# Optimization experiments

Measured on AMD Instinct MI355X. Metric: run time of the kernel, lower is better.

The kernel has to match this reference:

```python
import jax, jax.numpy as jnp
import numpy as np

TEMPERATURE = 8.0  # init arg


def setup_inputs() -> dict:
    key = jax.random.key(0)
    kq, kv, kk = jax.random.split(key, 3)
    B, W, H, C, M, D = 4, 64, 64, 256, 32, 32
    q = jax.random.normal(kq, (B, W, H, M, D), dtype=jnp.float32)
    v = jax.random.normal(kv, (B, W, H, C, M), dtype=jnp.float32)
    k = jax.random.normal(kk, (B, W, H, D, 1), dtype=jnp.float32)
    return {"q": q, "v": v, "k": k}


def reference(q, v, k):
    # attn = (q / T) @ k : [B,W,H,M,1]
    attn = jnp.matmul(q / TEMPERATURE, k)
    # softmax over dim=-2 (the query/slot axis M), NOT the usual key axis
    attn = jax.nn.softmax(attn, axis=-2)
    # v @ attn : [B,W,H,C,M] @ [B,W,H,M,1] -> [B,W,H,C,1] -> squeeze -> [B,W,H,C]
    out = jnp.matmul(v, attn)[..., 0]
    # permute(0,3,1,2) -> [B,C,W,H]; the subsequent .view is a no-op reshape
    return jnp.transpose(out, (0, 3, 1, 2))
```

## Files before the change

### kernel.cpp

```cpp
#include <hip/hip_runtime.h>


#define TEMP_INV 0.125f
#define G 16

typedef float f4 __attribute__((ext_vector_type(4)));

__global__ __launch_bounds__(256) void sdpa_kernel(
    const float* __restrict__ q,
    const float* __restrict__ v,
    const float* __restrict__ k,
    float* __restrict__ out)
{
    const int t   = threadIdx.x;
    const int p0  = blockIdx.x * G;
    const int b   = p0 >> 12;
    const int wh0 = p0 & 4095;

    __shared__ float s_k[G * 32];
    __shared__ float s_logit[G * 32];
    __shared__ float s_attn[G * 32];
    __shared__ float s_out[256 * 17];

    if (t < 128) {
        f4 k4 = ((const f4*)k)[p0 * 8 + t];
        k4 *= TEMP_INV;
        ((f4*)s_k)[t] = k4;
    }
    __syncthreads();

    const int j = t & 7;
    const int m = t >> 3;
    #pragma unroll 4
    for (int g = 0; g < G; ++g) {
        const f4 q4 = __builtin_nontemporal_load((const f4*)q + (p0 + g) * 256 + t);
        const float* kg = &s_k[g * 32 + j * 4];
        float partial = q4.x * kg[0] + q4.y * kg[1] + q4.z * kg[2] + q4.w * kg[3];
        partial += __shfl_down(partial, 4, 8);
        partial += __shfl_down(partial, 2, 8);
        partial += __shfl_down(partial, 1, 8);
        if (j == 0) s_logit[g * 32 + m] = partial;
    }
    __syncthreads();

    {
        const int mm = t & 31;
        #pragma unroll
        for (int r = 0; r < 2; ++r) {
            const int g = (t >> 5) + r * 8;
            float l = s_logit[g * 32 + mm];
            float mx = l;
            #pragma unroll
            for (int off = 16; off; off >>= 1)
                mx = fmaxf(mx, __shfl_xor(mx, off, 32));
            float e = __expf(l - mx);
            float s = e;
            #pragma unroll
            for (int off = 16; off; off >>= 1)
                s += __shfl_xor(s, off, 32);
            s_attn[g * 32 + mm] = e / s;
        }
    }
    __syncthreads();

    const int c0 = t >> 3;
    #pragma unroll 2
    for (int g = 0; g < G; ++g) {
        const float* ag = &s_attn[g * 32 + j * 4];
        const float a0 = ag[0], a1 = ag[1], a2 = ag[2], a3 = ag[3];
        const f4* v4p = (const f4*)v + (size_t)(p0 + g) * 2048;
        float acc[8];
        #pragma unroll
        for (int i = 0; i < 8; ++i) {
            const f4 v4 = __builtin_nontemporal_load(v4p + t + 256 * i);
            acc[i] = v4.x * a0 + v4.y * a1 + v4.z * a2 + v4.w * a3;
        }
        #pragma unroll
        for (int i = 0; i < 8; ++i) {
            acc[i] += __shfl_down(acc[i], 4, 8);
            acc[i] += __shfl_down(acc[i], 2, 8);
            acc[i] += __shfl_down(acc[i], 1, 8);
        }
        if (j == 0) {
            #pragma unroll
            for (int i = 0; i < 8; ++i)
                s_out[(c0 + 32 * i) * 17 + g] = acc[i];
        }
    }
    __syncthreads();

    {
        const int c  = t >> 2;
        const int gc = t & 3;
        #pragma unroll
        for (int i = 0; i < 4; ++i) {
            const int cc = c + 64 * i;
            const float* so = &s_out[cc * 17 + gc * 4];
            f4 o4 = { so[0], so[1], so[2], so[3] };
            __builtin_nontemporal_store(
                o4, (f4*)out + (size_t)(b * 256 + cc) * 1024 + (wh0 >> 2) + gc);
        }
    }
}

extern "C" void kernel_launch(void* const* d_in, const int* in_sizes, int n_in,
                              void* d_out, int out_size, void* d_ws, size_t ws_size,
                              hipStream_t stream) {
    const float* q = (const float*)d_in[0];
    const float* v = (const float*)d_in[1];
    const float* k = (const float*)d_in[2];
    float* out = (float*)d_out;
    sdpa_kernel<<<16384 / G, 256, 0, stream>>>(q, v, k, out);
}
```

Baseline: 683.5 us.

## Split fused kernel into attention kernel and channel-split PV kernel

Splits the single fused kernel into two launches. The first computes softmax attention weights and writes them to workspace. The second reads v with the grid split four ways over channels, so it launches four times as many blocks with a smaller per-thread load footprint and less shared memory. This aims to raise occupancy and memory parallelism on the dominant v stream, at the cost of an extra launch and a small round trip of attention weights through global memory.

```diff
diff --git a/kernel.cpp b/kernel.cpp
--- a/kernel.cpp
+++ b/kernel.cpp
@@ -3,24 +3,22 @@
 
 #define TEMP_INV 0.125f
 #define G 16
+#define CSPLIT 4
+#define CB (256 / CSPLIT)
 
 typedef float f4 __attribute__((ext_vector_type(4)));
 
-__global__ __launch_bounds__(256) void sdpa_kernel(
+__global__ __launch_bounds__(256) void attn_kernel(
     const float* __restrict__ q,
-    const float* __restrict__ v,
     const float* __restrict__ k,
-    float* __restrict__ out)
+    float* __restrict__ attn_out)
 {
-    const int t   = threadIdx.x;
-    const int p0  = blockIdx.x * G;
-    const int b   = p0 >> 12;
-    const int wh0 = p0 & 4095;
+    const int t  = threadIdx.x;
+    const int p0 = blockIdx.x * G;
 
     __shared__ float s_k[G * 32];
     __shared__ float s_logit[G * 32];
     __shared__ float s_attn[G * 32];
-    __shared__ float s_out[256 * 17];
 
     if (t < 128) {
         f4 k4 = ((const f4*)k)[p0 * 8 + t];
@@ -63,28 +61,49 @@
     }
     __syncthreads();
 
-    const int c0 = t >> 3;
-    #pragma unroll 2
+    if (t < 128)
+        ((f4*)attn_out)[p0 * 8 + t] = ((f4*)s_attn)[t];
+}
+
+__global__ __launch_bounds__(256) void pv_kernel(
+    const float* __restrict__ v,
+    const float* __restrict__ attn,
+    float* __restrict__ out)
+{
+    const int t   = threadIdx.x;
+    const int blk = blockIdx.x;
+    const int p0  = (blk >> 2) * G;
+    const int c0  = (blk & 3) * CB;
+    const int b   = p0 >> 12;
+    const int wh0 = p0 & 4095;
+
+    __shared__ float s_attn[G * 32];
+    __shared__ float s_out[CB * 17];
+
+    if (t < 128)
+        ((f4*)s_attn)[t] = ((const f4*)attn)[p0 * 8 + t];
+    __syncthreads();
+
+    const int j  = t & 7;
+    const int cr = t >> 3;
+    #pragma unroll 4
     for (int g = 0; g < G; ++g) {
         const float* ag = &s_attn[g * 32 + j * 4];
         const float a0 = ag[0], a1 = ag[1], a2 = ag[2], a3 = ag[3];
-        const f4* v4p = (const f4*)v + (size_t)(p0 + g) * 2048;
-        float acc[8];
-        #pragma unroll
-        for (int i = 0; i < 8; ++i) {
-            const f4 v4 = __builtin_nontemporal_load(v4p + t + 256 * i);
-            acc[i] = v4.x * a0 + v4.y * a1 + v4.z * a2 + v4.w * a3;
-        }
-        #pragma unroll
-        for (int i = 0; i < 8; ++i) {
-            acc[i] += __shfl_down(acc[i], 4, 8);
-            acc[i] += __shfl_down(acc[i], 2, 8);
-            acc[i] += __shfl_down(acc[i], 1, 8);
-        }
+        const f4* v4p = (const f4*)v + (size_t)(p0 + g) * 2048 + c0 * 8;
+        f4 v40 = __builtin_nontemporal_load(v4p + t);
+        f4 v41 = __builtin_nontemporal_load(v4p + t + 256);
+        float acc0 = v40.x * a0 + v40.y * a1 + v40.z * a2 + v40.w * a3;
+        float acc1 = v41.x * a0 + v41.y * a1 + v41.z * a2 + v41.w * a3;
+        acc0 += __shfl_down(acc0, 4, 8);
+        acc0 += __shfl_down(acc0, 2, 8);
+        acc0 += __shfl_down(acc0, 1, 8);
+        acc1 += __shfl_down(acc1, 4, 8);
+        acc1 += __shfl_down(acc1, 2, 8);
+        acc1 += __shfl_down(acc1, 1, 8);
         if (j == 0) {
-            #pragma unroll
-            for (int i = 0; i < 8; ++i)
-                s_out[(c0 + 32 * i) * 17 + g] = acc[i];
+            s_out[cr * 17 + g]        = acc0;
+            s_out[(cr + 32) * 17 + g] = acc1;
         }
     }
     __syncthreads();
@@ -92,14 +111,10 @@
     {
         const int c  = t >> 2;
         const int gc = t & 3;
-        #pragma unroll
-        for (int i = 0; i < 4; ++i) {
-            const int cc = c + 64 * i;
-            const float* so = &s_out[cc * 17 + gc * 4];
-            f4 o4 = { so[0], so[1], so[2], so[3] };
-            __builtin_nontemporal_store(
-                o4, (f4*)out + (size_t)(b * 256 + cc) * 1024 + (wh0 >> 2) + gc);
-        }
+        const float* so = &s_out[c * 17 + gc * 4];
+        f4 o4 = { so[0], so[1], so[2], so[3] };
+        __builtin_nontemporal_store(
+            o4, (f4*)out + (size_t)(b * 256 + c0 + c) * 1024 + (wh0 >> 2) + gc);
     }
 }
 
@@ -110,5 +125,8 @@
     const float* v = (const float*)d_in[1];
     const float* k = (const float*)d_in[2];
     float* out = (float*)d_out;
-    sdpa_kernel<<<16384 / G, 256, 0, stream>>>(q, v, k, out);
+    float* attn = (float*)d_ws;
+
+    attn_kernel<<<16384 / G, 256, 0, stream>>>(q, k, attn);
+    pv_kernel<<<(16384 / G) * CSPLIT, 256, 0, stream>>>(v, attn, out);
 }
```

Measured after the change: 689.5 us. About the same (+0.9%).

## Split into attention and PV kernels with per-thread full-row dot products

Applied to the files above, without the earlier changes.

Splits the fused kernel into two launches. The first computes the softmax attention weights into workspace, and the second computes the V-by-attention product. Each thread now loads a full 32-float row (8 consecutive f4) and does the whole dot product itself, which removes the shuffle reductions. The group per block also shrinks from 16 to 8 positions. In exchange there is an extra launch and a global round trip for the attention weights, loads are no longer coalesced across threads (each thread strides 128 bytes), and the nontemporal loads are dropped.

```diff
diff --git a/kernel.cpp b/kernel.cpp
--- a/kernel.cpp
+++ b/kernel.cpp
@@ -2,104 +2,95 @@
 
 
 #define TEMP_INV 0.125f
-#define G 16
 
 typedef float f4 __attribute__((ext_vector_type(4)));
 
-__global__ __launch_bounds__(256) void sdpa_kernel(
+__global__ __launch_bounds__(256) void attn_kernel(
     const float* __restrict__ q,
-    const float* __restrict__ v,
     const float* __restrict__ k,
-    float* __restrict__ out)
+    float* __restrict__ attn_out)
 {
-    const int t   = threadIdx.x;
-    const int p0  = blockIdx.x * G;
-    const int b   = p0 >> 12;
-    const int wh0 = p0 & 4095;
+    const int t  = threadIdx.x;
+    const int p0 = blockIdx.x * 8;
 
-    __shared__ float s_k[G * 32];
-    __shared__ float s_logit[G * 32];
-    __shared__ float s_attn[G * 32];
-    __shared__ float s_out[256 * 17];
+    __shared__ float s_k[8 * 32];
 
-    if (t < 128) {
+    if (t < 64) {
         f4 k4 = ((const f4*)k)[p0 * 8 + t];
         k4 *= TEMP_INV;
         ((f4*)s_k)[t] = k4;
     }
     __syncthreads();
 
-    const int j = t & 7;
-    const int m = t >> 3;
-    #pragma unroll 4
-    for (int g = 0; g < G; ++g) {
-        const f4 q4 = __builtin_nontemporal_load((const f4*)q + (p0 + g) * 256 + t);
-        const float* kg = &s_k[g * 32 + j * 4];
-        float partial = q4.x * kg[0] + q4.y * kg[1] + q4.z * kg[2] + q4.w * kg[3];
-        partial += __shfl_down(partial, 4, 8);
-        partial += __shfl_down(partial, 2, 8);
-        partial += __shfl_down(partial, 1, 8);
-        if (j == 0) s_logit[g * 32 + m] = partial;
+    const int g = t >> 5;
+    const int m = t & 31;
+
+    const f4* qp = (const f4*)q + ((size_t)(p0 + g) * 256 + m * 8);
+    const f4* kp = (const f4*)&s_k[g * 32];
+
+    float l = 0.f;
+    #pragma unroll
+    for (int i = 0; i < 8; ++i) {
+        const f4 qq = qp[i];
+        const f4 kk = kp[i];
+        l += qq.x * kk.x + qq.y * kk.y + qq.z * kk.z + qq.w * kk.w;
+    }
+
+    float mx = l;
+    #pragma unroll
+    for (int off = 16; off; off >>= 1)
+        mx = fmaxf(mx, __shfl_xor(mx, off, 32));
+    float e = __expf(l - mx);
+    float s = e;
+    #pragma unroll
+    for (int off = 16; off; off >>= 1)
+        s += __shfl_xor(s, off, 32);
+
+    attn_out[p0 * 32 + t] = e / s;
+}
+
+__global__ __launch_bounds__(256) void pv_kernel(
+    const float* __restrict__ v,
+    const float* __restrict__ attn,
+    float* __restrict__ out)
+{
+    const int t   = threadIdx.x;
+    const int p0  = blockIdx.x * 8;
+    const int b   = p0 >> 12;
+    const int wh0 = p0 & 4095;
+
+    __shared__ float s_attn[8 * 32];
+    __shared__ float s_out[256 * 9];
+
+    if (t < 64)
+        ((f4*)s_attn)[t] = ((const f4*)attn)[p0 * 8 + t];
+    __syncthreads();
+
+    const f4* vbase = (const f4*)v + ((size_t)p0 * 2048 + t * 8);
+    #pragma unroll
+    for (int g = 0; g < 8; ++g) {
+        const f4* vp = vbase + g * 2048;
+        const f4* ap = (const f4*)&s_attn[g * 32];
+        float a = 0.f;
+        #pragma unroll
+        for (int i = 0; i < 8; ++i) {
+            const f4 vv = vp[i];
+            const f4 aa = ap[i];
+            a += vv.x * aa.x + vv.y * aa.y + vv.z * aa.z + vv.w * aa.w;
+        }
+        s_out[t * 9 + g] = a;
     }
     __syncthreads();
 
-    {
-        const int mm = t & 31;
-        #pragma unroll
-        for (int r = 0; r < 2; ++r) {
-            const int g = (t >> 5) + r * 8;
-            float l = s_logit[g * 32 + mm];
-            float mx = l;
-            #pragma unroll
-            for (int off = 16; off; off >>= 1)
-                mx = fmaxf(mx, __shfl_xor(mx, off, 32));
-            float e = __expf(l - mx);
-            float s = e;
-            #pragma unroll
-            for (int off = 16; off; off >>= 1)
-                s += __shfl_xor(s, off, 32);
-            s_attn[g * 32 + mm] = e / s;
-        }
-    }
-    __syncthreads();
-
-    const int c0 = t >> 3;
-    #pragma unroll 2
-    for (int g = 0; g < G; ++g) {
-        const float* ag = &s_attn[g * 32 + j * 4];
-        const float a0 = ag[0], a1 = ag[1], a2 = ag[2], a3 = ag[3];
-        const f4* v4p = (const f4*)v + (size_t)(p0 + g) * 2048;
-        float acc[8];
-        #pragma unroll
-        for (int i = 0; i < 8; ++i) {
-            const f4 v4 = __builtin_nontemporal_load(v4p + t + 256 * i);
-            acc[i] = v4.x * a0 + v4.y * a1 + v4.z * a2 + v4.w * a3;
-        }
-        #pragma unroll
-        for (int i = 0; i < 8; ++i) {
-            acc[i] += __shfl_down(acc[i], 4, 8);
-            acc[i] += __shfl_down(acc[i], 2, 8);
-            acc[i] += __shfl_down(acc[i], 1, 8);
-        }
-        if (j == 0) {
-            #pragma unroll
-            for (int i = 0; i < 8; ++i)
-                s_out[(c0 + 32 * i) * 17 + g] = acc[i];
-        }
-    }
-    __syncthreads();
-
-    {
-        const int c  = t >> 2;
-        const int gc = t & 3;
-        #pragma unroll
-        for (int i = 0; i < 4; ++i) {
-            const int cc = c + 64 * i;
-            const float* so = &s_out[cc * 17 + gc * 4];
-            f4 o4 = { so[0], so[1], so[2], so[3] };
-            __builtin_nontemporal_store(
-                o4, (f4*)out + (size_t)(b * 256 + cc) * 1024 + (wh0 >> 2) + gc);
-        }
+    #pragma unroll
+    for (int i = 0; i < 2; ++i) {
+        const int f  = i * 256 + t;
+        const int c  = f >> 1;
+        const int gc = f & 1;
+        const float* so = &s_out[c * 9 + gc * 4];
+        f4 o4 = { so[0], so[1], so[2], so[3] };
+        __builtin_nontemporal_store(
+            o4, (f4*)out + (size_t)(b * 256 + c) * 1024 + (wh0 >> 2) + gc);
     }
 }
 
@@ -110,5 +101,8 @@
     const float* v = (const float*)d_in[1];
     const float* k = (const float*)d_in[2];
     float* out = (float*)d_out;
-    sdpa_kernel<<<16384 / G, 256, 0, stream>>>(q, v, k, out);
+    float* attn = (float*)d_ws;
+
+    attn_kernel<<<16384 / 8, 256, 0, stream>>>(q, k, attn);
+    pv_kernel<<<16384 / 8, 256, 0, stream>>>(v, attn, out);
 }
```

New measurement: 741.2 us. 8.4% more time.
